# Kernel optimization log

Measured on AMD Instinct MI355X. Metric: run time of the kernel, lower is better.

## Reference

```python
import jax, jax.numpy as jnp
import numpy as np

N, K, D = 131072, 1024, 128


def setup_inputs() -> dict:
    key = jax.random.key(0)
    k1, k2 = jax.random.split(key)
    latent = jax.random.normal(k1, (N, D), dtype=jnp.float32)
    coords = jax.random.uniform(k2, (K, D), dtype=jnp.float32)  # torch.rand init
    return {"latent": latent, "coords": coords}


def reference(latent, coords):
    # Euclidean cdist argmin: sqrt is monotone, so argmin of squared distances
    # matches torch.cdist(...).min(1)[1].
    x2 = jnp.sum(latent * latent, axis=1, keepdims=True)          # [N, 1]
    c2 = jnp.sum(coords * coords, axis=1)[None, :]                # [1, K]
    d2 = x2 + c2 - 2.0 * (latent @ coords.T)                      # [N, K]
    closest_centroid = jnp.argmin(d2, axis=1)                     # [N] int
    # original also computes cluster_distances but discards it; output is indices
    return closest_centroid
```

## Files before the change

### kernel.cpp

```cpp
#include <hip/hip_runtime.h>


constexpr int N = 131072;
constexpr int K = 1024;
constexpr int D = 128;

typedef __attribute__((ext_vector_type(8))) _Float16 half8;
typedef __attribute__((ext_vector_type(4))) float f32x4;

typedef const __attribute__((address_space(1))) uint* gas_uint;
typedef __attribute__((address_space(3))) uint* las_uint;

union UH { uint4 u; half8 h; };
__device__ inline half8 as_h8(uint4 v) { UH x; x.u = v; return x.h; }

union H2U { _Float16 h[2]; uint u; };
__device__ inline uint fp16pk(float a, float b) {
    H2U x;
    x.h[0] = (_Float16)a;
    x.h[1] = (_Float16)b;
    return x.u;
}
__device__ inline void fp16split(float a, _Float16& hi, _Float16& lo) {
    hi = (_Float16)a;
    lo = (_Float16)(a - (float)hi);
}
__device__ inline void pk2(float a, float b, uint& h, uint& l) {
    _Float16 ha, la, hb, lb;
    fp16split(a, ha, la);
    fp16split(b, hb, lb);
    H2U x, y;
    x.h[0] = ha; x.h[1] = hb;
    y.h[0] = la; y.h[1] = lb;
    h = x.u;
    l = y.u;
}

__global__ __launch_bounds__(256) void prep_kernel(
    const float* __restrict__ coords, float* __restrict__ c2half,
    uint* __restrict__ chi, int* __restrict__ counter) {
    if (blockIdx.x == 0 && threadIdx.x == 0) counter[0] = 0;
    const int k = blockIdx.x * 4 + (threadIdx.x >> 6);
    const int dw = threadIdx.x & 63;
    float a = coords[k * D + 2 * dw], b = coords[k * D + 2 * dw + 1];
    const int g = dw >> 2, sub = dw & 3, kt = k >> 4, m = k & 15;
    char* base = (char*)chi + (size_t)kt * 4096 + m * 256 +
                 ((g ^ m) << 4) + sub * 4;
    *(uint*)base = fp16pk(a, b);
    float s = fmaf(a, a, b * b);
#pragma unroll
    for (int off = 1; off < 64; off <<= 1) s += __shfl_xor(s, off);
    if (dw == 0) c2half[k] = 0.5f * s;
}

__global__ __launch_bounds__(256) void transpose_kernel(
    const float* __restrict__ coords, float* __restrict__ coordsT) {
    __shared__ float tile[64][65];
    const int k0 = blockIdx.x * 64;
    const int d0 = blockIdx.y * 64;
    const int tx = threadIdx.x & 63, ty = threadIdx.x >> 6;
#pragma unroll
    for (int i = 0; i < 64; i += 4)
        tile[ty + i][tx] = coords[(size_t)(k0 + ty + i) * D + d0 + tx];
    __syncthreads();
#pragma unroll
    for (int i = 0; i < 64; i += 4)
        coordsT[(size_t)(d0 + ty + i) * K + k0 + tx] = tile[tx][ty + i];
}

__global__ __launch_bounds__(256, 4) void centroid_mfma_kernel(
    const float* __restrict__ latent, const uint* __restrict__ chi,
    const float* __restrict__ c2, int* __restrict__ out,
    int* __restrict__ counter, int* __restrict__ list) {
    __shared__ __align__(16) char smem[36864];
    const int l = threadIdx.x & 63, w = threadIdx.x >> 6;
    const int l15 = l & 15, l4 = l >> 4;
    const int rowbase = blockIdx.x * 128 + w * 32;
    char* const wbuf = smem + w * 8192;

    uint4 bh[2][4], bl[2][4];
    float n2[2];
#pragma unroll
    for (int grp = 0; grp < 2; ++grp) {
        const float* rp =
            latent + (size_t)(rowbase + grp * 16 + l15) * D + l4 * 8;
        float s2 = 0.f;
#pragma unroll
        for (int s = 0; s < 4; ++s) {
            float4 u = *(const float4*)(rp + 32 * s);
            float4 v = *(const float4*)(rp + 32 * s + 4);
            s2 += u.x * u.x + u.y * u.y + u.z * u.z + u.w * u.w +
                  v.x * v.x + v.y * v.y + v.z * v.z + v.w * v.w;
            uint h0, o0, h1, o1, h2, o2, h3, o3;
            pk2(-u.x, -u.y, h0, o0);
            pk2(-u.z, -u.w, h1, o1);
            pk2(-v.x, -v.y, h2, o2);
            pk2(-v.z, -v.w, h3, o3);
            bh[grp][s] = make_uint4(h0, h1, h2, h3);
            bl[grp][s] = make_uint4(o0, o1, o2, o3);
        }
        n2[grp] = s2;
    }
#pragma unroll
    for (int grp = 0; grp < 2; ++grp) {
        n2[grp] += __shfl_xor(n2[grp], 16);
        n2[grp] += __shfl_xor(n2[grp], 32);
    }

    {
        float4* dst = (float4*)(smem + 32768);
        const float4* src = (const float4*)c2;
#pragma unroll
        for (int i = 0; i < 4; ++i) dst[i * 64 + l] = src[i * 64 + l];
    }

    const char* gsrc0 = (const char*)chi + (l << 4);
#pragma unroll
    for (int i = 0; i < 4; ++i)
        __builtin_amdgcn_global_load_lds((gas_uint)(gsrc0 + i * 1024),
                                         (las_uint)(wbuf + i * 1024), 16, 0, 0);
#pragma unroll
    for (int i = 0; i < 4; ++i)
        __builtin_amdgcn_global_load_lds((gas_uint)(gsrc0 + 4096 + i * 1024),
                                         (las_uint)(wbuf + 4096 + i * 1024),
                                         16, 0, 0);

    float m1[2] = {3.4e38f, 3.4e38f};
    float m2[2] = {3.4e38f, 3.4e38f};
    const float* c2l = (const float*)(smem + 32768);
    float4 cq = *(const float4*)(c2l + l4 * 4);

#pragma unroll 1
    for (int t = 0; t < 64; ++t) {
        const int buf = t & 1;
        if (t < 63)
            asm volatile("s_waitcnt vmcnt(4)" ::: "memory");
        else
            asm volatile("s_waitcnt vmcnt(0)" ::: "memory");
        __builtin_amdgcn_sched_barrier(0);

        f32x4 acc[2];
#pragma unroll
        for (int grp = 0; grp < 2; ++grp) {
            acc[grp][0] = cq.x;
            acc[grp][1] = cq.y;
            acc[grp][2] = cq.z;
            acc[grp][3] = cq.w;
        }
        if (t + 1 < 64) cq = *(const float4*)(c2l + (t + 1) * 16 + l4 * 4);

        const char* lhs = wbuf + buf * 4096;
        __builtin_amdgcn_s_setprio(1);
#pragma unroll
        for (int s = 0; s < 4; ++s) {
            half8 a = *(const half8*)(lhs + l15 * 256 + (((l4 + 4 * s) ^ l15) << 4));
            acc[0] = __builtin_amdgcn_mfma_f32_16x16x32_f16(a, as_h8(bh[0][s]),
                                                            acc[0], 0, 0, 0);
            acc[1] = __builtin_amdgcn_mfma_f32_16x16x32_f16(a, as_h8(bh[1][s]),
                                                            acc[1], 0, 0, 0);
            acc[0] = __builtin_amdgcn_mfma_f32_16x16x32_f16(a, as_h8(bl[0][s]),
                                                            acc[0], 0, 0, 0);
            acc[1] = __builtin_amdgcn_mfma_f32_16x16x32_f16(a, as_h8(bl[1][s]),
                                                            acc[1], 0, 0, 0);
        }
        __builtin_amdgcn_s_setprio(0);
        __builtin_amdgcn_sched_barrier(0);

        const uint kbase = ((uint)t << 4) + l4 * 4;
#pragma unroll
        for (int r = 0; r < 4; ++r) {
#pragma unroll
            for (int grp = 0; grp < 2; ++grp) {
                uint pb = (__float_as_uint(acc[grp][r]) & 0xFFFFFC00u) |
                          (kbase + r);
                float vp = __uint_as_float(pb);
                m2[grp] = __builtin_amdgcn_fmed3f(vp, m1[grp], m2[grp]);
                m1[grp] = fminf(m1[grp], vp);
            }
        }

        asm volatile("s_waitcnt lgkmcnt(0)" ::: "memory");
        __builtin_amdgcn_sched_barrier(0);
        if (t < 62) {
            const char* gs = gsrc0 + (size_t)(t + 2) * 4096;
            char* ls = wbuf + buf * 4096;
#pragma unroll
            for (int i = 0; i < 4; ++i)
                __builtin_amdgcn_global_load_lds((gas_uint)(gs + i * 1024),
                                                 (las_uint)(ls + i * 1024),
                                                 16, 0, 0);
        }
    }

#pragma unroll
    for (int off = 16; off <= 32; off <<= 1) {
#pragma unroll
        for (int grp = 0; grp < 2; ++grp) {
            float om = __shfl_xor(m1[grp], off);
            float o2 = __shfl_xor(m2[grp], off);
            m2[grp] = fminf(fminf(m2[grp], o2), fmaxf(m1[grp], om));
            m1[grp] = fminf(m1[grp], om);
        }
    }

    bool flg[2];
    unsigned long long bm[2];
    int total = 0;
#pragma unroll
    for (int grp = 0; grp < 2; ++grp) {
        float eps = 0.0028f * sqrtf(n2[grp]) + 0.015f;
        flg[grp] = (l < 16) && ((m2[grp] - m1[grp]) <= eps);
        bm[grp] = __ballot(flg[grp]);
        total += __popcll(bm[grp]);
    }
    int pos = 0;
    if (l == 0 && total) pos = atomicAdd(counter, total);
    pos = __shfl(pos, 0);
    if (l < 16) {
        int run = pos;
#pragma unroll
        for (int grp = 0; grp < 2; ++grp) {
            out[rowbase + grp * 16 + l] = (int)(__float_as_uint(m1[grp]) & 1023u);
            if (flg[grp])
                list[run + __popcll(bm[grp] & ((1ull << l) - 1ull))] =
                    rowbase + grp * 16 + l;
            run += __popcll(bm[grp]);
        }
    }
}

__global__ __launch_bounds__(256) void centroid_exact_kernel(
    const float* __restrict__ latent, const float* __restrict__ coordsT,
    const float* __restrict__ c2, const int* __restrict__ cnt_list,
    int* __restrict__ out) {
    const int count = cnt_list[0];
    const int* list = cnt_list + 16;
    const int lane = threadIdx.x & 63;
    const int gw = (blockIdx.x * 256 + threadIdx.x) >> 6;
    const int nwaves = gridDim.x * 4;

    for (int task = gw; task * 4 < count; task += nwaves) {
        const int base = task * 4;
        const int nr = min(4, count - base);
        const float* xp[4];
        int rows[4];
#pragma unroll
        for (int j = 0; j < 4; ++j) {
            int idx = base + (j < nr ? j : nr - 1);
            rows[j] = __builtin_amdgcn_readfirstlane(list[idx]);
            xp[j] = latent + (size_t)rows[j] * D;
        }

        float acc[16][4];
#pragma unroll
        for (int c = 0; c < 16; ++c) {
            float cc = c2[c * 64 + lane];
#pragma unroll
            for (int j = 0; j < 4; ++j) acc[c][j] = cc;
        }

#pragma unroll 1
        for (int d4 = 0; d4 < D / 4; ++d4) {
            float4 xq[4];
#pragma unroll
            for (int j = 0; j < 4; ++j)
                xq[j] = *(const float4*)(xp[j] + 4 * d4);
            float ct[4][16];
#pragma unroll
            for (int dd = 0; dd < 4; ++dd)
#pragma unroll
                for (int c = 0; c < 16; ++c)
                    ct[dd][c] = coordsT[(size_t)(4 * d4 + dd) * K + c * 64 + lane];
#pragma unroll
            for (int dd = 0; dd < 4; ++dd) {
#pragma unroll
                for (int c = 0; c < 16; ++c) {
#pragma unroll
                    for (int j = 0; j < 4; ++j) {
                        float xv = (dd == 0) ? xq[j].x
                                 : (dd == 1) ? xq[j].y
                                 : (dd == 2) ? xq[j].z : xq[j].w;
                        acc[c][j] = fmaf(-xv, ct[dd][c], acc[c][j]);
                    }
                }
            }
        }

#pragma unroll
        for (int j = 0; j < 4; ++j) {
            float m1 = acc[0][j];
            int i1 = lane;
#pragma unroll
            for (int c = 1; c < 16; ++c) {
                const int kk = c * 64 + lane;
                if (acc[c][j] < m1) { m1 = acc[c][j]; i1 = kk; }
            }
#pragma unroll
            for (int off = 1; off < 64; off <<= 1) {
                float om = __shfl_xor(m1, off);
                int oi = __shfl_xor(i1, off);
                if (om < m1 || (om == m1 && oi < i1)) { m1 = om; i1 = oi; }
            }
            if (lane == 0 && j < nr) out[rows[j]] = i1;
        }
    }
}

extern "C" void kernel_launch(void* const* d_in, const int* in_sizes, int n_in,
                              void* d_out, int out_size, void* d_ws, size_t ws_size,
                              hipStream_t stream) {
    const float* latent = (const float*)d_in[0];
    const float* coords = (const float*)d_in[1];
    int* out = (int*)d_out;

    char* ws = (char*)d_ws;
    size_t off = 0;
    float* c2 = (float*)(ws + off); off += 4096;
    uint* chi = (uint*)(ws + off); off += 262144;
    float* coordsT = (float*)(ws + off); off += 524288;
    int* cnt_list = (int*)(ws + off); off += 64 + 524288;
    int* counter = cnt_list;
    int* list = cnt_list + 16;

    prep_kernel<<<K / 4, 256, 0, stream>>>(coords, c2, chi, counter);
    {
        dim3 g(K / 64, D / 64);
        transpose_kernel<<<g, 256, 0, stream>>>(coords, coordsT);
    }
    centroid_mfma_kernel<<<N / 128, 256, 0, stream>>>(latent, chi, c2, out,
                                                      counter, list);
    centroid_exact_kernel<<<2048, 256, 0, stream>>>(latent, coordsT, c2,
                                                    cnt_list, out);
}
```

Baseline: 145.4 us.

## Read c2 from global, prefetch next tile before argmin update

Drops the LDS staging of the centroid norms c2 and loads each tile's c2 values straight from global memory, which also shrinks the shared-memory allocation. The async global-to-LDS prefetch of tile t+2 is now issued right after the MFMAs instead of after the min/second-min update, so the next copy starts earlier. Both accumulators now start from a shared init vector instead of separate per-group copies. In exchange, a global load now sits inside the loop's vmcnt accounting, and each tile's c2 value depends on global/cache latency.

```diff
diff --git a/kernel.cpp b/kernel.cpp
--- a/kernel.cpp
+++ b/kernel.cpp
@@ -72,7 +72,7 @@
     const float* __restrict__ latent, const uint* __restrict__ chi,
     const float* __restrict__ c2, int* __restrict__ out,
     int* __restrict__ counter, int* __restrict__ list) {
-    __shared__ __align__(16) char smem[36864];
+    __shared__ __align__(16) char smem[32768];
     const int l = threadIdx.x & 63, w = threadIdx.x >> 6;
     const int l15 = l & 15, l4 = l >> 4;
     const int rowbase = blockIdx.x * 128 + w * 32;
@@ -107,13 +107,6 @@
         n2[grp] += __shfl_xor(n2[grp], 32);
     }
 
-    {
-        float4* dst = (float4*)(smem + 32768);
-        const float4* src = (const float4*)c2;
-#pragma unroll
-        for (int i = 0; i < 4; ++i) dst[i * 64 + l] = src[i * 64 + l];
-    }
-
     const char* gsrc0 = (const char*)chi + (l << 4);
 #pragma unroll
     for (int i = 0; i < 4; ++i)
@@ -127,8 +120,7 @@
 
     float m1[2] = {3.4e38f, 3.4e38f};
     float m2[2] = {3.4e38f, 3.4e38f};
-    const float* c2l = (const float*)(smem + 32768);
-    float4 cq = *(const float4*)(c2l + l4 * 4);
+    float4 cq = *(const float4*)(c2 + l4 * 4);
 
 #pragma unroll 1
     for (int t = 0; t < 64; ++t) {
@@ -139,20 +131,29 @@
             asm volatile("s_waitcnt vmcnt(0)" ::: "memory");
         __builtin_amdgcn_sched_barrier(0);
 
+        f32x4 cinit;
+        cinit[0] = cq.x;
+        cinit[1] = cq.y;
+        cinit[2] = cq.z;
+        cinit[3] = cq.w;
+        if (t + 1 < 64) cq = *(const float4*)(c2 + (t + 1) * 16 + l4 * 4);
+
+        const char* lhs = wbuf + buf * 4096;
         f32x4 acc[2];
-#pragma unroll
-        for (int grp = 0; grp < 2; ++grp) {
-            acc[grp][0] = cq.x;
-            acc[grp][1] = cq.y;
-            acc[grp][2] = cq.z;
-            acc[grp][3] = cq.w;
-        }
-        if (t + 1 < 64) cq = *(const float4*)(c2l + (t + 1) * 16 + l4 * 4);
-
-        const char* lhs = wbuf + buf * 4096;
         __builtin_amdgcn_s_setprio(1);
-#pragma unroll
-        for (int s = 0; s < 4; ++s) {
+        {
+            half8 a0 = *(const half8*)(lhs + l15 * 256 + ((l4 ^ l15) << 4));
+            acc[0] = __builtin_amdgcn_mfma_f32_16x16x32_f16(a0, as_h8(bh[0][0]),
+                                                            cinit, 0, 0, 0);
+            acc[1] = __builtin_amdgcn_mfma_f32_16x16x32_f16(a0, as_h8(bh[1][0]),
+                                                            cinit, 0, 0, 0);
+            acc[0] = __builtin_amdgcn_mfma_f32_16x16x32_f16(a0, as_h8(bl[0][0]),
+                                                            acc[0], 0, 0, 0);
+            acc[1] = __builtin_amdgcn_mfma_f32_16x16x32_f16(a0, as_h8(bl[1][0]),
+                                                            acc[1], 0, 0, 0);
+        }
+#pragma unroll
+        for (int s = 1; s < 4; ++s) {
             half8 a = *(const half8*)(lhs + l15 * 256 + (((l4 + 4 * s) ^ l15) << 4));
             acc[0] = __builtin_amdgcn_mfma_f32_16x16x32_f16(a, as_h8(bh[0][s]),
                                                             acc[0], 0, 0, 0);
@@ -166,6 +167,18 @@
         __builtin_amdgcn_s_setprio(0);
         __builtin_amdgcn_sched_barrier(0);
 
+        asm volatile("s_waitcnt lgkmcnt(0)" ::: "memory");
+        __builtin_amdgcn_sched_barrier(0);
+        if (t < 62) {
+            const char* gs = gsrc0 + (size_t)(t + 2) * 4096;
+            char* ls = wbuf + buf * 4096;
+#pragma unroll
+            for (int i = 0; i < 4; ++i)
+                __builtin_amdgcn_global_load_lds((gas_uint)(gs + i * 1024),
+                                                 (las_uint)(ls + i * 1024),
+                                                 16, 0, 0);
+        }
+
         const uint kbase = ((uint)t << 4) + l4 * 4;
 #pragma unroll
         for (int r = 0; r < 4; ++r) {
@@ -177,18 +190,6 @@
                 m2[grp] = __builtin_amdgcn_fmed3f(vp, m1[grp], m2[grp]);
                 m1[grp] = fminf(m1[grp], vp);
             }
-        }
-
-        asm volatile("s_waitcnt lgkmcnt(0)" ::: "memory");
-        __builtin_amdgcn_sched_barrier(0);
-        if (t < 62) {
-            const char* gs = gsrc0 + (size_t)(t + 2) * 4096;
-            char* ls = wbuf + buf * 4096;
-#pragma unroll
-            for (int i = 0; i < 4; ++i)
-                __builtin_amdgcn_global_load_lds((gas_uint)(gs + i * 1024),
-                                                 (las_uint)(ls + i * 1024),
-                                                 16, 0, 0);
         }
     }
 
```

After: 146.1 us. No clear change (+0.5%).
